# Kernel optimization log

Measured on AMD Instinct MI355X. Metric: run time of the kernel, lower is better.

## Reference

```python
import jax, jax.numpy as jnp
import numpy as np

N, C, H, K = 32768, 128, 4, 16
D = C // H  # head_dim = 32


def setup_inputs() -> dict:
    key = jax.random.key(0)
    ks = jax.random.split(key, 8)
    feats = jax.random.normal(ks[0], (N, C), dtype=jnp.float32)
    coords = jax.random.normal(ks[1], (N, 3), dtype=jnp.float32)
    knn_idx = jax.random.randint(ks[2], (N, K), 0, N, dtype=jnp.int64)
    s = 0.02
    Wq = jax.random.normal(ks[3], (C, C), dtype=jnp.float32) * s
    Wk = jax.random.normal(ks[4], (C, C), dtype=jnp.float32) * s
    Wv = jax.random.normal(ks[5], (C, C), dtype=jnp.float32) * s
    Wo = jax.random.normal(ks[6], (C, C), dtype=jnp.float32) * s
    bo = jnp.zeros((C,), dtype=jnp.float32)
    return {"feats": feats, "coords": coords, "knn_idx": knn_idx,
            "Wq": Wq, "Wk": Wk, "Wv": Wv, "Wo": Wo, "bo": bo}


def reference(feats, coords, knn_idx, Wq, Wk, Wv, Wo, bo):
    # coords only feeds the kNN search (precomputed as knn_idx)
    n, c = feats.shape
    q = (feats @ Wq.T).reshape(n, H, D)          # [N,H,D]
    k = (feats @ Wk.T).reshape(n, H, D)          # [N,H,D]
    v = (feats @ Wv.T).reshape(n, H, D)          # [N,H,D]
    kn = k[knn_idx]                               # gather -> [N,K,H,D]
    vn = v[knn_idx]                               # gather -> [N,K,H,D]
    scores = jnp.einsum('nhd,nkhd->nhk', q, kn) / jnp.sqrt(jnp.float32(D))
    w = jax.nn.softmax(scores, axis=-1)           # softmax over K neighbors
    out = jnp.einsum('nhk,nkhd->nhd', w, vn).reshape(n, c)
    return out @ Wo.T + bo
```

## Files before the change

kernel.cpp:

```cpp
#include <hip/hip_runtime.h>

#define NPTS 32768
#define C 128
#define KNBR 16

typedef __attribute__((ext_vector_type(8))) short short8;
typedef __attribute__((ext_vector_type(4))) float floatx4;
typedef __attribute__((ext_vector_type(4))) int intx4;

__device__ __forceinline__ ushort f2b(float f) {
    union { float f; uint u; } x; x.f = f;
    uint r = (x.u + 0x7fffu + ((x.u >> 16) & 1u)) >> 16;
    return (ushort)r;
}
__device__ __forceinline__ ushort f2h(float f) {
    union { _Float16 h; ushort u; } x; x.h = (_Float16)f; return x.u;
}
__device__ __forceinline__ float h2f(ushort u) {
    union { ushort u; _Float16 h; } x; x.u = u; return (float)x.h;
}

__device__ __forceinline__ int col_of(int w, int b) {
    return 64 * (w >> 4) + 32 * ((w >> 3) & 1) + 16 * (b & 1) + 2 * (w & 7) + (b >> 1);
}

__global__ __launch_bounds__(256) void prep_all(
    const float* __restrict__ feats, const float* __restrict__ Wq,
    const float* __restrict__ Wk, const float* __restrict__ Wv,
    const float* __restrict__ Wo,
    ushort* __restrict__ feats_b, ushort* __restrict__ wq_b,
    ushort* __restrict__ wk_b, ushort* __restrict__ wv_b, ushort* __restrict__ wo_b)
{
    const int b = blockIdx.x, tid = threadIdx.x;
    if (b < 2048 + 24) {
        const float* src; ushort* dst; size_t base;
        if (b < 2048) { src = feats; dst = feats_b; base = (size_t)b * 2048; }
        else {
            const int wb = b - 2048, wsel = wb >> 3;
            base = (size_t)(wb & 7) * 2048;
            src = (wsel == 0) ? Wq : (wsel == 1) ? Wk : Wv;
            dst = (wsel == 0) ? wq_b : (wsel == 1) ? wk_b : wv_b;
        }
        const size_t i = base + (size_t)tid * 8;
        float4 v0 = *(const float4*)(src + i);
        float4 v1 = *(const float4*)(src + i + 4);
        intx4 o;
        o.x = (int)((uint)f2b(v0.x) | ((uint)f2b(v0.y) << 16));
        o.y = (int)((uint)f2b(v0.z) | ((uint)f2b(v0.w) << 16));
        o.z = (int)((uint)f2b(v1.x) | ((uint)f2b(v1.y) << 16));
        o.w = (int)((uint)f2b(v1.z) | ((uint)f2b(v1.w) << 16));
        *(intx4*)(dst + i) = o;
    } else {
        const int wb = b - 2072;
        const size_t i = (size_t)wb * 2048 + (size_t)tid * 8;
        ushort tmp[8];
#pragma unroll
        for (int t = 0; t < 8; ++t) {
            const int gi = (int)(i + t);
            const int j = gi >> 7, s = gi & 127;
            tmp[t] = f2b(Wo[(size_t)j * 128 + col_of(s >> 2, s & 3)]);
        }
        intx4 o;
        o.x = (int)((uint)tmp[0] | ((uint)tmp[1] << 16));
        o.y = (int)((uint)tmp[2] | ((uint)tmp[3] << 16));
        o.z = (int)((uint)tmp[4] | ((uint)tmp[5] << 16));
        o.w = (int)((uint)tmp[6] | ((uint)tmp[7] << 16));
        *(intx4*)(wo_b + i) = o;
    }
}

__device__ __forceinline__ void stage128_b(const ushort* __restrict__ gsrc, ushort* lds, int tid)
{
#pragma unroll
    for (int it = 0; it < 8; ++it) {
        const int f = it * 256 + tid;
        const int row = f >> 4, slot = f & 15;
        intx4 v = *(const intx4*)(gsrc + (size_t)f * 8);
        *(intx4*)(lds + ((row * 16 + (slot ^ (row & 7))) * 8)) = v;
    }
}

__device__ __forceinline__ void gemm_frag_acc(const ushort* ldsA, const ushort* ldsW,
                                              floatx4 acc[4][4], int lane)
{
    const int fr = lane & 15, kb = lane >> 4;
#pragma unroll
    for (int kk = 0; kk < 4; ++kk) {
        const int slot = kk * 4 + kb;
        short8 af[4], bf[4];
#pragma unroll
        for (int i = 0; i < 4; ++i) {
            const int row = i * 16 + fr;
            af[i] = *(const short8*)(ldsA + ((row * 16 + (slot ^ (row & 7))) * 8));
            bf[i] = *(const short8*)(ldsW + ((row * 16 + (slot ^ (row & 7))) * 8));
        }
#pragma unroll
        for (int i = 0; i < 4; ++i)
#pragma unroll
            for (int j = 0; j < 4; ++j)
                acc[i][j] = __builtin_amdgcn_mfma_f32_16x16x32_bf16(af[i], bf[j], acc[i][j], 0, 0, 0);
    }
}

__global__ __launch_bounds__(256) void qkv_gemm(
    const ushort* __restrict__ A, const ushort* __restrict__ wq_b,
    const ushort* __restrict__ wk_b, const ushort* __restrict__ wv_b,
    unsigned char* __restrict__ q8, unsigned char* __restrict__ kv8,
    ushort* __restrict__ scpack, float* __restrict__ qscale)
{
    __shared__ ushort ldsA[16384];
    __shared__ ushort ldsW[16384];
    __shared__ float rmax[2][128];
    const int tid = threadIdx.x, lane = tid & 63, wid = tid >> 6;
    const int r0 = blockIdx.x * 128, sel = blockIdx.y;
    const ushort* W = (sel == 0) ? wq_b : (sel == 1) ? wk_b : wv_b;

    stage128_b(A + (size_t)r0 * 128, ldsA, tid);
    stage128_b(W, ldsW, tid);
    __syncthreads();

    floatx4 acc[4][4];
#pragma unroll
    for (int i = 0; i < 4; ++i)
#pragma unroll
        for (int j = 0; j < 4; ++j) acc[i][j] = (floatx4){0.f, 0.f, 0.f, 0.f};

    const int wr = (wid >> 1) * 64, wc = (wid & 1) * 64;
    gemm_frag_acc(ldsA + wr * 16 * 8, ldsW + wc * 16 * 8, acc, lane);

    const int fr = lane & 15, kb = lane >> 4;

    float mx[4][4];
#pragma unroll
    for (int i = 0; i < 4; ++i)
#pragma unroll
        for (int r = 0; r < 4; ++r) {
            float m = fabsf(acc[i][0][r]);
            m = fmaxf(m, fabsf(acc[i][1][r]));
            m = fmaxf(m, fabsf(acc[i][2][r]));
            m = fmaxf(m, fabsf(acc[i][3][r]));
            m = fmaxf(m, __shfl_xor(m, 1));
            m = fmaxf(m, __shfl_xor(m, 2));
            m = fmaxf(m, __shfl_xor(m, 4));
            m = fmaxf(m, __shfl_xor(m, 8));
            mx[i][r] = m;
        }
    if (fr == 0) {
#pragma unroll
        for (int i = 0; i < 4; ++i)
#pragma unroll
            for (int r = 0; r < 4; ++r)
                rmax[wc >> 6][wr + i * 16 + kb * 4 + r] = mx[i][r];
    }
    __syncthreads();

    const int boff = ((wc >> 5) + (fr & 1)) * 32 + (fr >> 1) * 4;
#pragma unroll
    for (int i = 0; i < 4; ++i)
#pragma unroll
        for (int r = 0; r < 4; ++r) {
            const int lr = wr + i * 16 + kb * 4 + r;
            const int nn = r0 + lr;
            const float comb = fmaxf(fmaxf(rmax[0][lr], rmax[1][lr]), 1e-20f);
            const float qs = 127.f / comb;
            int b0 = __float2int_rn(acc[i][0][r] * qs);
            int b1 = __float2int_rn(acc[i][1][r] * qs);
            int b2 = __float2int_rn(acc[i][2][r] * qs);
            int b3 = __float2int_rn(acc[i][3][r] * qs);
            uint u_lo = (uint)(b0 & 0xff) | ((uint)(b1 & 0xff) << 8);
            uint u_hi = (uint)(b2 & 0xff) | ((uint)(b3 & 0xff) << 8);
            uint o_lo = __shfl_xor(u_lo, 1);
            uint o_hi = __shfl_xor(u_hi, 1);
            uint word = (fr & 1) ? (o_hi | (u_hi << 16)) : (u_lo | (o_lo << 16));
            if (sel == 0) {
                *(uint*)(q8 + (size_t)nn * 128 + boff) = word;
                if (fr == 0 && wc == 0) qscale[nn] = comb * (1.f / 127.f);
            } else if (sel == 1) {
                *(uint*)(kv8 + (size_t)nn * 256 + boff) = word;
                if (fr == 0 && wc == 0) scpack[(size_t)nn * 2] = f2h(comb * (1.f / 127.f));
            } else {
                *(uint*)(kv8 + (size_t)nn * 256 + 128 + boff) = word;
                if (fr == 0 && wc == 0) scpack[(size_t)nn * 2 + 1] = f2h(comb * (1.f / 127.f));
            }
        }
}

__global__ __launch_bounds__(256, 6) void attn_kernel(
    const unsigned char* __restrict__ q8, const unsigned char* __restrict__ kv8,
    const ushort* __restrict__ scpack, const float* __restrict__ qscale,
    const int* __restrict__ knn, ushort* __restrict__ attn_p)
{
    const int tid = threadIdx.x;
    const int lane = tid & 63;
    const int wp = __builtin_amdgcn_readfirstlane(tid >> 6);
    const int n = blockIdx.x * 4 + wp;

    const int kk = lane >> 2, h = lane & 3;
    const int nb4 = knn[(size_t)n * KNBR + kk];
    const int* kr = knn + (size_t)n * KNBR;

    const unsigned char* krow = kv8 + (size_t)nb4 * 256 + h * 32;
    intx4 k0 = *(const intx4*)(krow);
    intx4 k1 = *(const intx4*)(krow + 16);
    const unsigned char* qrow = q8 + (size_t)n * 128 + h * 32;
    intx4 qq0 = *(const intx4*)(qrow);
    intx4 qq1 = *(const intx4*)(qrow + 16);
    const uint scp = *(const uint*)(scpack + (size_t)nb4 * 2);

    ushort vsh[KNBR];
#pragma unroll
    for (int j = 0; j < KNBR; ++j) {
        const int nbv = kr[j];
        vsh[j] = *(const ushort*)(kv8 + (size_t)nbv * 256 + 128 + lane * 2);
    }

    const float qs6 = qscale[n] * 0.17677669529663687f;

    int dp = 0;
#if __has_builtin(__builtin_amdgcn_sdot4)
#pragma unroll
    for (int i = 0; i < 4; ++i) dp = __builtin_amdgcn_sdot4(qq0[i], k0[i], dp, false);
#pragma unroll
    for (int i = 0; i < 4; ++i) dp = __builtin_amdgcn_sdot4(qq1[i], k1[i], dp, false);
#else
#pragma unroll
    for (int i = 0; i < 4; ++i) {
        uint a = (uint)qq0[i], b = (uint)k0[i];
        dp += (int)(signed char)(a) * (int)(signed char)(b)
            + (int)(signed char)(a >> 8) * (int)(signed char)(b >> 8)
            + (int)(signed char)(a >> 16) * (int)(signed char)(b >> 16)
            + (int)(signed char)(a >> 24) * (int)(signed char)(b >> 24);
        a = (uint)qq1[i]; b = (uint)k1[i];
        dp += (int)(signed char)(a) * (int)(signed char)(b)
            + (int)(signed char)(a >> 8) * (int)(signed char)(b >> 8)
            + (int)(signed char)(a >> 16) * (int)(signed char)(b >> 16)
            + (int)(signed char)(a >> 24) * (int)(signed char)(b >> 24);
    }
#endif

    const float ksc = h2f((ushort)(scp & 0xffff));
    const float vsc = h2f((ushort)(scp >> 16));
    const float sc = (float)dp * ksc * qs6;

    float mxv = sc;
    mxv = fmaxf(mxv, __shfl_xor(mxv, 4));
    mxv = fmaxf(mxv, __shfl_xor(mxv, 8));
    mxv = fmaxf(mxv, __shfl_xor(mxv, 16));
    mxv = fmaxf(mxv, __shfl_xor(mxv, 32));
    const float e = __expf(sc - mxv);
    float sm = e;
    sm += __shfl_xor(sm, 4);
    sm += __shfl_xor(sm, 8);
    sm += __shfl_xor(sm, 16);
    sm += __shfl_xor(sm, 32);
    const float wgt = e * vsc / sm;

    const int h2v = lane >> 4;
    float a0 = 0.f, a1 = 0.f;
#pragma unroll
    for (int j = 0; j < KNBR; ++j) {
        const float w2 = __shfl(wgt, j * 4 + h2v);
        const ushort u = vsh[j];
        a0 += w2 * (float)(signed char)(u & 0xff);
        a1 += w2 * (float)(signed char)(u >> 8);
    }
    const uint pr = (uint)f2b(a0) | ((uint)f2b(a1) << 16);
    *(uint*)(attn_p + (size_t)n * 128 + lane * 2) = pr;
}

__global__ __launch_bounds__(256) void out_gemm(
    const ushort* __restrict__ A, const ushort* __restrict__ wo_b,
    const float* __restrict__ bias, float* __restrict__ out)
{
    __shared__ ushort ldsA[16384];
    __shared__ ushort ldsW[16384];
    const int tid = threadIdx.x, lane = tid & 63, wid = tid >> 6;
    const int r0 = blockIdx.x * 128;

    stage128_b(A + (size_t)r0 * 128, ldsA, tid);
    stage128_b(wo_b, ldsW, tid);
    __syncthreads();

    floatx4 acc[4][4];
#pragma unroll
    for (int i = 0; i < 4; ++i)
#pragma unroll
        for (int j = 0; j < 4; ++j) acc[i][j] = (floatx4){0.f, 0.f, 0.f, 0.f};

    const int wr = (wid >> 1) * 64, wc = (wid & 1) * 64;
    gemm_frag_acc(ldsA + wr * 16 * 8, ldsW + wc * 16 * 8, acc, lane);

    const int fr = lane & 15, kb = lane >> 4;
#pragma unroll
    for (int i = 0; i < 4; ++i)
#pragma unroll
        for (int j = 0; j < 4; ++j) {
            const int col = wc + j * 16 + fr;
            const float bv = bias[col];
#pragma unroll
            for (int r = 0; r < 4; ++r) {
                const int n = r0 + wr + i * 16 + kb * 4 + r;
                out[(size_t)n * 128 + col] = acc[i][j][r] + bv;
            }
        }
}

extern "C" void kernel_launch(void* const* d_in, const int* in_sizes, int n_in,
                              void* d_out, int out_size, void* d_ws, size_t ws_size,
                              hipStream_t stream)
{
    const float* feats = (const float*)d_in[0];
    const int*   knn   = (const int*)d_in[2];
    const float* Wq    = (const float*)d_in[3];
    const float* Wk    = (const float*)d_in[4];
    const float* Wv    = (const float*)d_in[5];
    const float* Wo    = (const float*)d_in[6];
    const float* bo    = (const float*)d_in[7];
    float* out = (float*)d_out;

    ushort* attn_p  = (ushort*)d_ws;
    ushort* feats_b = attn_p + (size_t)NPTS * C;
    unsigned char* q8  = (unsigned char*)(feats_b + (size_t)NPTS * C);
    unsigned char* kv8 = q8 + (size_t)NPTS * 128;
    ushort* scpack = (ushort*)(kv8 + (size_t)NPTS * 256);
    float* qscale  = (float*)(scpack + (size_t)NPTS * 2);
    ushort* wq_b   = (ushort*)(qscale + (size_t)NPTS);
    ushort* wk_b   = wq_b + 16384;
    ushort* wv_b   = wk_b + 16384;
    ushort* wo_b   = wv_b + 16384;

    prep_all<<<2080, 256, 0, stream>>>(feats, Wq, Wk, Wv, Wo,
                                       feats_b, wq_b, wk_b, wv_b, wo_b);
    qkv_gemm<<<dim3(NPTS / 128, 3), 256, 0, stream>>>(feats_b, wq_b, wk_b, wv_b,
                                                      q8, kv8, scpack, qscale);
    attn_kernel<<<NPTS / 4, 256, 0, stream>>>(q8, kv8, scpack, qscale, knn, attn_p);
    out_gemm<<<NPTS / 128, 256, 0, stream>>>(attn_p, wo_b, bo, out);
}
```

Before: 49.42 us.

## Fuse neighbor attention with output projection GEMM in one kernel

Merges the attention kernel and the output projection GEMM into a single 512-thread kernel. Each wave computes attention for 8 points and writes bf16 results straight into swizzled LDS, and the block then runs a 64x128 MFMA GEMM against Wo staged in LDS. This removes the global attn_p round trip and one launch. Because the attention output is now stored in natural column order, the Wo prep no longer needs its column permutation and goes through the plain conversion path. In exchange there are far fewer blocks (512 instead of 8192) and each wave processes points serially, which may reduce latency hiding for the random kNN gathers.

```diff
diff --git a/kernel.cpp b/kernel.cpp
--- a/kernel.cpp
+++ b/kernel.cpp
@@ -32,41 +32,23 @@
     ushort* __restrict__ wk_b, ushort* __restrict__ wv_b, ushort* __restrict__ wo_b)
 {
     const int b = blockIdx.x, tid = threadIdx.x;
-    if (b < 2048 + 24) {
-        const float* src; ushort* dst; size_t base;
-        if (b < 2048) { src = feats; dst = feats_b; base = (size_t)b * 2048; }
-        else {
-            const int wb = b - 2048, wsel = wb >> 3;
-            base = (size_t)(wb & 7) * 2048;
-            src = (wsel == 0) ? Wq : (wsel == 1) ? Wk : Wv;
-            dst = (wsel == 0) ? wq_b : (wsel == 1) ? wk_b : wv_b;
-        }
-        const size_t i = base + (size_t)tid * 8;
-        float4 v0 = *(const float4*)(src + i);
-        float4 v1 = *(const float4*)(src + i + 4);
-        intx4 o;
-        o.x = (int)((uint)f2b(v0.x) | ((uint)f2b(v0.y) << 16));
-        o.y = (int)((uint)f2b(v0.z) | ((uint)f2b(v0.w) << 16));
-        o.z = (int)((uint)f2b(v1.x) | ((uint)f2b(v1.y) << 16));
-        o.w = (int)((uint)f2b(v1.z) | ((uint)f2b(v1.w) << 16));
-        *(intx4*)(dst + i) = o;
-    } else {
-        const int wb = b - 2072;
-        const size_t i = (size_t)wb * 2048 + (size_t)tid * 8;
-        ushort tmp[8];
-#pragma unroll
-        for (int t = 0; t < 8; ++t) {
-            const int gi = (int)(i + t);
-            const int j = gi >> 7, s = gi & 127;
-            tmp[t] = f2b(Wo[(size_t)j * 128 + col_of(s >> 2, s & 3)]);
-        }
-        intx4 o;
-        o.x = (int)((uint)tmp[0] | ((uint)tmp[1] << 16));
-        o.y = (int)((uint)tmp[2] | ((uint)tmp[3] << 16));
-        o.z = (int)((uint)tmp[4] | ((uint)tmp[5] << 16));
-        o.w = (int)((uint)tmp[6] | ((uint)tmp[7] << 16));
-        *(intx4*)(wo_b + i) = o;
-    }
+    const float* src; ushort* dst; size_t base;
+    if (b < 2048) { src = feats; dst = feats_b; base = (size_t)b * 2048; }
+    else {
+        const int wb = b - 2048, wsel = wb >> 3;
+        base = (size_t)(wb & 7) * 2048;
+        src = (wsel == 0) ? Wq : (wsel == 1) ? Wk : (wsel == 2) ? Wv : Wo;
+        dst = (wsel == 0) ? wq_b : (wsel == 1) ? wk_b : (wsel == 2) ? wv_b : wo_b;
+    }
+    const size_t i = base + (size_t)tid * 8;
+    float4 v0 = *(const float4*)(src + i);
+    float4 v1 = *(const float4*)(src + i + 4);
+    intx4 o;
+    o.x = (int)((uint)f2b(v0.x) | ((uint)f2b(v0.y) << 16));
+    o.y = (int)((uint)f2b(v0.z) | ((uint)f2b(v0.w) << 16));
+    o.z = (int)((uint)f2b(v1.x) | ((uint)f2b(v1.y) << 16));
+    o.w = (int)((uint)f2b(v1.z) | ((uint)f2b(v1.w) << 16));
+    *(intx4*)(dst + i) = o;
 }
 
 __device__ __forceinline__ void stage128_b(const ushort* __restrict__ gsrc, ushort* lds, int tid)
@@ -185,124 +167,139 @@
         }
 }
 
-__global__ __launch_bounds__(256, 6) void attn_kernel(
+__global__ __launch_bounds__(512) void fused_attn_out(
     const unsigned char* __restrict__ q8, const unsigned char* __restrict__ kv8,
     const ushort* __restrict__ scpack, const float* __restrict__ qscale,
-    const int* __restrict__ knn, ushort* __restrict__ attn_p)
-{
-    const int tid = threadIdx.x;
-    const int lane = tid & 63;
-    const int wp = __builtin_amdgcn_readfirstlane(tid >> 6);
-    const int n = blockIdx.x * 4 + wp;
+    const int* __restrict__ knn, const ushort* __restrict__ wo_b,
+    const float* __restrict__ bias, float* __restrict__ out)
+{
+    __shared__ ushort ldsW[16384];
+    __shared__ ushort ldsA[8192];
+    const int tid = threadIdx.x, lane = tid & 63, wid = tid >> 6;
+    const int p0 = blockIdx.x * 64;
+
+#pragma unroll
+    for (int it = 0; it < 4; ++it) {
+        const int f = it * 512 + tid;
+        const int row = f >> 4, slot = f & 15;
+        intx4 v = *(const intx4*)(wo_b + (size_t)f * 8);
+        *(intx4*)(ldsW + ((row * 16 + (slot ^ (row & 7))) * 8)) = v;
+    }
 
     const int kk = lane >> 2, h = lane & 3;
-    const int nb4 = knn[(size_t)n * KNBR + kk];
-    const int* kr = knn + (size_t)n * KNBR;
-
-    const unsigned char* krow = kv8 + (size_t)nb4 * 256 + h * 32;
-    intx4 k0 = *(const intx4*)(krow);
-    intx4 k1 = *(const intx4*)(krow + 16);
-    const unsigned char* qrow = q8 + (size_t)n * 128 + h * 32;
-    intx4 qq0 = *(const intx4*)(qrow);
-    intx4 qq1 = *(const intx4*)(qrow + 16);
-    const uint scp = *(const uint*)(scpack + (size_t)nb4 * 2);
-
-    ushort vsh[KNBR];
-#pragma unroll
-    for (int j = 0; j < KNBR; ++j) {
-        const int nbv = kr[j];
-        vsh[j] = *(const ushort*)(kv8 + (size_t)nbv * 256 + 128 + lane * 2);
-    }
-
-    const float qs6 = qscale[n] * 0.17677669529663687f;
-
-    int dp = 0;
+    const int h2v = lane >> 4;
+    const int cb = 32 * (lane >> 4) + (lane & 15);
+
+#pragma unroll
+    for (int p = 0; p < 8; ++p) {
+        const int n = p0 + wid * 8 + p;
+        const int* kr = knn + (size_t)n * KNBR;
+        const int nb4 = kr[kk];
+
+        const unsigned char* krow = kv8 + (size_t)nb4 * 256 + h * 32;
+        intx4 k0 = *(const intx4*)(krow);
+        intx4 k1 = *(const intx4*)(krow + 16);
+        const unsigned char* qrow = q8 + (size_t)n * 128 + h * 32;
+        intx4 qq0 = *(const intx4*)(qrow);
+        intx4 qq1 = *(const intx4*)(qrow + 16);
+        const uint scp = *(const uint*)(scpack + (size_t)nb4 * 2);
+
+        ushort vsh[KNBR];
+#pragma unroll
+        for (int j = 0; j < KNBR; ++j) {
+            const int nbv = kr[j];
+            vsh[j] = *(const ushort*)(kv8 + (size_t)nbv * 256 + 128 + lane * 2);
+        }
+
+        const float qs6 = qscale[n] * 0.17677669529663687f;
+
+        int dp = 0;
 #if __has_builtin(__builtin_amdgcn_sdot4)
 #pragma unroll
-    for (int i = 0; i < 4; ++i) dp = __builtin_amdgcn_sdot4(qq0[i], k0[i], dp, false);
-#pragma unroll
-    for (int i = 0; i < 4; ++i) dp = __builtin_amdgcn_sdot4(qq1[i], k1[i], dp, false);
+        for (int i = 0; i < 4; ++i) dp = __builtin_amdgcn_sdot4(qq0[i], k0[i], dp, false);
+#pragma unroll
+        for (int i = 0; i < 4; ++i) dp = __builtin_amdgcn_sdot4(qq1[i], k1[i], dp, false);
 #else
 #pragma unroll
-    for (int i = 0; i < 4; ++i) {
-        uint a = (uint)qq0[i], b = (uint)k0[i];
-        dp += (int)(signed char)(a) * (int)(signed char)(b)
-            + (int)(signed char)(a >> 8) * (int)(signed char)(b >> 8)
-            + (int)(signed char)(a >> 16) * (int)(signed char)(b >> 16)
-            + (int)(signed char)(a >> 24) * (int)(signed char)(b >> 24);
-        a = (uint)qq1[i]; b = (uint)k1[i];
-        dp += (int)(signed char)(a) * (int)(signed char)(b)
-            + (int)(signed char)(a >> 8) * (int)(signed char)(b >> 8)
-            + (int)(signed char)(a >> 16) * (int)(signed char)(b >> 16)
-            + (int)(signed char)(a >> 24) * (int)(signed char)(b >> 24);
-    }
+        for (int i = 0; i < 4; ++i) {
+            uint a = (uint)qq0[i], b = (uint)k0[i];
+            dp += (int)(signed char)(a) * (int)(signed char)(b)
+                + (int)(signed char)(a >> 8) * (int)(signed char)(b >> 8)
+                + (int)(signed char)(a >> 16) * (int)(signed char)(b >> 16)
+                + (int)(signed char)(a >> 24) * (int)(signed char)(b >> 24);
+            a = (uint)qq1[i]; b = (uint)k1[i];
+            dp += (int)(signed char)(a) * (int)(signed char)(b)
+                + (int)(signed char)(a >> 8) * (int)(signed char)(b >> 8)
+                + (int)(signed char)(a >> 16) * (int)(signed char)(b >> 16)
+                + (int)(signed char)(a >> 24) * (int)(signed char)(b >> 24);
+        }
 #endif
 
-    const float ksc = h2f((ushort)(scp & 0xffff));
-    const float vsc = h2f((ushort)(scp >> 16));
-    const float sc = (float)dp * ksc * qs6;
-
-    float mxv = sc;
-    mxv = fmaxf(mxv, __shfl_xor(mxv, 4));
-    mxv = fmaxf(mxv, __shfl_xor(mxv, 8));
-    mxv = fmaxf(mxv, __shfl_xor(mxv, 16));
-    mxv = fmaxf(mxv, __shfl_xor(mxv, 32));
-    const float e = __expf(sc - mxv);
-    float sm = e;
-    sm += __shfl_xor(sm, 4);
-    sm += __shfl_xor(sm, 8);
-    sm += __shfl_xor(sm, 16);
-    sm += __shfl_xor(sm, 32);
-    const float wgt = e * vsc / sm;
-
-    const int h2v = lane >> 4;
-    float a0 = 0.f, a1 = 0.f;
-#pragma unroll
-    for (int j = 0; j < KNBR; ++j) {
-        const float w2 = __shfl(wgt, j * 4 + h2v);
-        const ushort u = vsh[j];
-        a0 += w2 * (float)(signed char)(u & 0xff);
-        a1 += w2 * (float)(signed char)(u >> 8);
-    }
-    const uint pr = (uint)f2b(a0) | ((uint)f2b(a1) << 16);
-    *(uint*)(attn_p + (size_t)n * 128 + lane * 2) = pr;
-}
-
-__global__ __launch_bounds__(256) void out_gemm(
-    const ushort* __restrict__ A, const ushort* __restrict__ wo_b,
-    const float* __restrict__ bias, float* __restrict__ out)
-{
-    __shared__ ushort ldsA[16384];
-    __shared__ ushort ldsW[16384];
-    const int tid = threadIdx.x, lane = tid & 63, wid = tid >> 6;
-    const int r0 = blockIdx.x * 128;
-
-    stage128_b(A + (size_t)r0 * 128, ldsA, tid);
-    stage128_b(wo_b, ldsW, tid);
+        const float ksc = h2f((ushort)(scp & 0xffff));
+        const float vsc = h2f((ushort)(scp >> 16));
+        const float sc = (float)dp * ksc * qs6;
+
+        float mxv = sc;
+        mxv = fmaxf(mxv, __shfl_xor(mxv, 4));
+        mxv = fmaxf(mxv, __shfl_xor(mxv, 8));
+        mxv = fmaxf(mxv, __shfl_xor(mxv, 16));
+        mxv = fmaxf(mxv, __shfl_xor(mxv, 32));
+        const float e = __expf(sc - mxv);
+        float sm = e;
+        sm += __shfl_xor(sm, 4);
+        sm += __shfl_xor(sm, 8);
+        sm += __shfl_xor(sm, 16);
+        sm += __shfl_xor(sm, 32);
+        const float wgt = e * vsc / sm;
+
+        float a0 = 0.f, a1 = 0.f;
+#pragma unroll
+        for (int j = 0; j < KNBR; ++j) {
+            const float w2 = __shfl(wgt, j * 4 + h2v);
+            const ushort u = vsh[j];
+            a0 += w2 * (float)(signed char)(u & 0xff);
+            a1 += w2 * (float)(signed char)(u >> 8);
+        }
+        const int row = wid * 8 + p;
+        const int s0 = cb >> 3, s1 = (cb + 16) >> 3;
+        ldsA[(row * 16 + (s0 ^ (row & 7))) * 8 + (cb & 7)] = f2b(a0);
+        ldsA[(row * 16 + (s1 ^ (row & 7))) * 8 + ((cb + 16) & 7)] = f2b(a1);
+    }
     __syncthreads();
 
-    floatx4 acc[4][4];
-#pragma unroll
-    for (int i = 0; i < 4; ++i)
-#pragma unroll
-        for (int j = 0; j < 4; ++j) acc[i][j] = (floatx4){0.f, 0.f, 0.f, 0.f};
-
-    const int wr = (wid >> 1) * 64, wc = (wid & 1) * 64;
-    gemm_frag_acc(ldsA + wr * 16 * 8, ldsW + wc * 16 * 8, acc, lane);
-
     const int fr = lane & 15, kb = lane >> 4;
-#pragma unroll
-    for (int i = 0; i < 4; ++i)
+    const int wr = (wid & 3) * 16, wc = (wid >> 2) * 64;
+
+    floatx4 acc[4];
+#pragma unroll
+    for (int j = 0; j < 4; ++j) acc[j] = (floatx4){0.f, 0.f, 0.f, 0.f};
+
+#pragma unroll
+    for (int kkk = 0; kkk < 4; ++kkk) {
+        const int slot = kkk * 4 + kb;
+        const int arow = wr + fr;
+        short8 af = *(const short8*)(ldsA + ((arow * 16 + (slot ^ (arow & 7))) * 8));
+        short8 bf[4];
 #pragma unroll
         for (int j = 0; j < 4; ++j) {
-            const int col = wc + j * 16 + fr;
-            const float bv = bias[col];
-#pragma unroll
-            for (int r = 0; r < 4; ++r) {
-                const int n = r0 + wr + i * 16 + kb * 4 + r;
-                out[(size_t)n * 128 + col] = acc[i][j][r] + bv;
-            }
-        }
+            const int brow = wc + j * 16 + fr;
+            bf[j] = *(const short8*)(ldsW + ((brow * 16 + (slot ^ (brow & 7))) * 8));
+        }
+#pragma unroll
+        for (int j = 0; j < 4; ++j)
+            acc[j] = __builtin_amdgcn_mfma_f32_16x16x32_bf16(af, bf[j], acc[j], 0, 0, 0);
+    }
+
+#pragma unroll
+    for (int j = 0; j < 4; ++j) {
+        const int col = wc + j * 16 + fr;
+        const float bv = bias[col];
+#pragma unroll
+        for (int r = 0; r < 4; ++r) {
+            const int n = p0 + wr + kb * 4 + r;
+            out[(size_t)n * 128 + col] = acc[j][r] + bv;
+        }
+    }
 }
 
 extern "C" void kernel_launch(void* const* d_in, const int* in_sizes, int n_in,
@@ -318,8 +315,7 @@
     const float* bo    = (const float*)d_in[7];
     float* out = (float*)d_out;
 
-    ushort* attn_p  = (ushort*)d_ws;
-    ushort* feats_b = attn_p + (size_t)NPTS * C;
+    ushort* feats_b = (ushort*)d_ws;
     unsigned char* q8  = (unsigned char*)(feats_b + (size_t)NPTS * C);
     unsigned char* kv8 = q8 + (size_t)NPTS * 128;
     ushort* scpack = (ushort*)(kv8 + (size_t)NPTS * 256);
@@ -333,6 +329,6 @@
                                        feats_b, wq_b, wk_b, wv_b, wo_b);
     qkv_gemm<<<dim3(NPTS / 128, 3), 256, 0, stream>>>(feats_b, wq_b, wk_b, wv_b,
                                                       q8, kv8, scpack, qscale);
-    attn_kernel<<<NPTS / 4, 256, 0, stream>>>(q8, kv8, scpack, qscale, knn, attn_p);
-    out_gemm<<<NPTS / 128, 256, 0, stream>>>(attn_p, wo_b, bo, out);
-}
+    fused_attn_out<<<NPTS / 64, 512, 0, stream>>>(q8, kv8, scpack, qscale, knn,
+                                                  wo_b, bo, out);
+}
```

New measurement: 49.48 us. Within noise of the previous version (+0.1%).
